# Kernel optimization log

Hardware: AMD Instinct MI355X
Metric: run time of the kernel (lower is better)

## Reference

```python
import jax, jax.numpy as jnp
import numpy as np

D_MODEL = 2048
NUM_HEADS = 16
NUM_KV_HEADS = 4
HEAD_DIM = D_MODEL // NUM_HEADS  # 128
B, T = 2, 2048


def setup_inputs() -> dict:
    key = jax.random.key(0)
    ks = jax.random.split(key, 9)
    d_kv = NUM_KV_HEADS * HEAD_DIM
    s = 1.0 / np.sqrt(D_MODEL)
    return {
        "x": jax.random.normal(ks[0], (B, T, D_MODEL), dtype=jnp.float32),
        "Wq": jax.random.normal(ks[1], (D_MODEL, D_MODEL), dtype=jnp.float32) * s,
        "bq": jnp.zeros((D_MODEL,), dtype=jnp.float32),
        "Wk": jax.random.normal(ks[2], (D_MODEL, d_kv), dtype=jnp.float32) * s,
        "bk": jnp.zeros((d_kv,), dtype=jnp.float32),
        "Wv": jax.random.normal(ks[3], (D_MODEL, d_kv), dtype=jnp.float32) * s,
        "bv": jnp.zeros((d_kv,), dtype=jnp.float32),
        "Wo": jax.random.normal(ks[4], (D_MODEL, D_MODEL), dtype=jnp.float32) * s,
        "bo": jnp.zeros((D_MODEL,), dtype=jnp.float32),
    }


def reference(x, Wq, bq, Wk, bk, Wv, bv, Wo, bo):
    b, t, _ = x.shape
    # projections
    q = x @ Wq + bq                      # [B,T,D]
    k = x @ Wk + bk                      # [B,T,KVH*Dh]
    v = x @ Wv + bv
    q = q.reshape(b, t, NUM_HEADS, HEAD_DIM)      # [B,T,H,Dh]
    k = k.reshape(b, t, NUM_KV_HEADS, HEAD_DIM)   # [B,T,KVH,Dh]
    v = v.reshape(b, t, NUM_KV_HEADS, HEAD_DIM)
    repeat = NUM_HEADS // NUM_KV_HEADS
    k = jnp.repeat(k, repeat, axis=2)              # [B,T,H,Dh]
    v = jnp.repeat(v, repeat, axis=2)
    scores = jnp.einsum('bthd,bshd->bhts', q, k) / jnp.sqrt(
        jnp.asarray(HEAD_DIM, dtype=x.dtype))
    mask = jnp.tril(jnp.ones((t, t), dtype=x.dtype))
    # faithful to source: multiplicative mask plus large negative on masked
    scores = scores * mask - 1e10 * (1.0 - mask)
    probs = jax.nn.softmax(scores, axis=-1)        # [B,H,T,S]
    out = jnp.einsum('bhts,bshd->bthd', probs, v)  # [B,T,H,Dh]
    out = out.reshape(b, t, NUM_HEADS * HEAD_DIM)  # merge heads
    return out @ Wo + bo                           # [B,T,D]
```

## Files before the change

### kernel.cpp

```cpp
#include <hip/hip_runtime.h>

typedef __attribute__((ext_vector_type(8))) __bf16 bf16x8;
typedef __attribute__((ext_vector_type(4))) float f32x4;
typedef __attribute__((ext_vector_type(4))) short short4v;

#define MFMA16(a,b,c)  __builtin_amdgcn_mfma_f32_16x16x32_bf16((a),(b),(c),0,0,0)
#define MFMA16K(a,b,c) __builtin_amdgcn_mfma_f32_16x16x16bf16_1k((a),(b),(c),0,0,0)

__device__ __forceinline__ short f2bf(float f){
  union { float f; unsigned u; } x; x.f = f;
  return (short)((x.u + 0x7fffu + ((x.u >> 16) & 1u)) >> 16);
}
__device__ __forceinline__ unsigned bits(float f){
  union { float f; unsigned u; } x; x.f = f; return x.u;
}

__device__ __forceinline__ void gld16(void* lds, const void* g){
  __builtin_amdgcn_global_load_lds(
      (const __attribute__((address_space(1))) unsigned*)g,
      (__attribute__((address_space(3))) unsigned*)lds, 16, 0, 0);
}


__global__ __launch_bounds__(256) void k_cvt8(const float* __restrict__ x,
                                              short* __restrict__ xb){
  long i = (long)blockIdx.x * 256 + threadIdx.x;
  const float4* xv = (const float4*)x;
  float4 a = xv[2*i], c = xv[2*i+1];
  short s[8] = {f2bf(a.x),f2bf(a.y),f2bf(a.z),f2bf(a.w),
                f2bf(c.x),f2bf(c.y),f2bf(c.z),f2bf(c.w)};
  *(uint4*)&xb[8*i] = *(uint4*)s;
}

__global__ void k_wt(const float* __restrict__ W, short* __restrict__ Wt, int N){
  __shared__ float tile[32][33];
  int tx = threadIdx.x, ty = threadIdx.y;
  int k0 = blockIdx.y*32, n0 = blockIdx.x*32;
  for (int j=0;j<32;j+=8)
    tile[ty+j][tx] = W[(size_t)(k0+ty+j)*N + n0 + tx];
  __syncthreads();
  for (int j=0;j<32;j+=8)
    Wt[(size_t)(n0+ty+j)*2048 + k0 + tx] = f2bf(tile[tx][ty+j]);
}

__global__ void k_bias(const float* __restrict__ bq, const float* __restrict__ bk,
                       const float* __restrict__ bv, float* __restrict__ outb){
  int i = blockIdx.x*256 + threadIdx.x;
  float v = (i < 2048) ? bq[i] : (i < 2560 ? bk[i-2048] : bv[i-2560]);
  outb[i] = v;
}

__global__ void k_vt(const short* __restrict__ qkv, short* __restrict__ Vt){
  __shared__ short tile[32][33];
  int tx = threadIdx.x, ty = threadIdx.y;
  int t0 = blockIdx.x*32, c0 = blockIdx.y*32;
  for (int j=0;j<32;j+=8)
    tile[ty+j][tx] = qkv[(size_t)(t0+ty+j)*3072 + 2560 + c0 + tx];
  __syncthreads();
  int b = t0 >> 11, t_in_b = t0 & 2047;
  for (int j=0;j<32;j+=8){
    int col = c0 + ty + j;
    int kvh = col >> 7, d = col & 127;
    Vt[((size_t)((b*4 + kvh)*128 + d))*2048 + t_in_b + tx] = tile[tx][ty+j];
  }
}

template<int OUT_BF16>
__global__ __launch_bounds__(256) void gemm_bt(const short* __restrict__ A,
    const short* __restrict__ Bt, const float* __restrict__ bias,
    void* __restrict__ Cv, int M, int N, int K){
  __shared__ short As[128*32];
  __shared__ short Bs[128*32];
  const int tid = threadIdx.x;
  const int w = tid >> 6, lane = tid & 63, l15 = lane & 15, quad = lane >> 4;
  const int wr = w >> 1, wc = w & 1;
  const int nbx = gridDim.x;
  const int lin = blockIdx.y * nbx + blockIdx.x;
  const int cpx = (nbx * gridDim.y) >> 3;
  const int swz = (lin & 7) * cpx + (lin >> 3);
  const int m0 = (swz / nbx) * 128, n0 = (swz % nbx) * 128;
  const int lrow = lane >> 2, lcol = (lane & 3)*8;
  const short* Ag = A  + (size_t)(m0 + w*32 + lrow)*K + lcol;
  const short* Bg = Bt + (size_t)(n0 + w*32 + lrow)*K + lcol;
  short* AsW0 = &As[(w*32)*32];
  short* AsW1 = &As[(w*32+16)*32];
  short* BsW0 = &Bs[(w*32)*32];
  short* BsW1 = &Bs[(w*32+16)*32];
  const size_t r16K = (size_t)16*K;
  f32x4 acc[4][4] = {};
  for (int kt = 0; kt < K; kt += 32){
    gld16(AsW0, Ag + kt);
    gld16(AsW1, Ag + kt + r16K);
    gld16(BsW0, Bg + kt);
    gld16(BsW1, Bg + kt + r16K);
    __syncthreads();
    bf16x8 af[4], bfr[4];
#pragma unroll
    for (int i=0;i<4;i++){
      af[i]  = *(const bf16x8*)&As[(wr*64 + i*16 + l15)*32 + quad*8];
      bfr[i] = *(const bf16x8*)&Bs[(wc*64 + i*16 + l15)*32 + quad*8];
    }
#pragma unroll
    for (int mi=0;mi<4;mi++)
#pragma unroll
      for (int nj=0;nj<4;nj++)
        acc[mi][nj] = MFMA16(af[mi], bfr[nj], acc[mi][nj]);
    __syncthreads();
  }
  float bv[4];
#pragma unroll
  for (int nj=0;nj<4;nj++) bv[nj] = bias[n0 + wc*64 + nj*16 + l15];
#pragma unroll
  for (int mi=0;mi<4;mi++){
    int row = m0 + wr*64 + mi*16 + quad*4;
#pragma unroll
    for (int nj=0;nj<4;nj++){
      int col = n0 + wc*64 + nj*16 + l15;
#pragma unroll
      for (int r=0;r<4;r++){
        float v = acc[mi][nj][r] + bv[nj];
        if (OUT_BF16) ((short*)Cv)[(size_t)(row+r)*N + col] = f2bf(v);
        else          ((float*)Cv)[(size_t)(row+r)*N + col] = v;
      }
    }
  }
}

__global__ __launch_bounds__(256) void k_attn(const short* __restrict__ qkv,
                                              const short* __restrict__ Vt,
                                              short* __restrict__ attn){
  constexpr float COEF = 0.12752365f;
  __shared__ short SM[16384];
  const int tid = threadIdx.x, w = tid >> 6, lane = tid & 63;
  const int l15 = lane & 15, quad = lane >> 4;
  const int p = blockIdx.x, h = blockIdx.y, b = blockIdx.z, kvh = h >> 2;

  const short* kb[2];
  const short* vb[2];
#pragma unroll
  for (int j=0;j<2;j++){
    int rK = w*8 + j*4 + (lane >> 4);
    int cK = (lane & 15) ^ (rK & 15);
    kb[j] = qkv + (size_t)(b*2048 + rK)*3072 + 2048 + kvh*128 + cK*8;
    int dV = w*32 + j*16 + (lane >> 2);
    int cV = (lane & 3) ^ (dV & 3) ^ ((dV >> 2) & 3);
    vb[j] = Vt + ((size_t)((b*4 + kvh)*128 + dV))*2048 + cV*8;
  }
  short* K0 = &SM[w*1024];
  short* V0 = &SM[4096 + w*1024];

  int buf = 0;
#pragma unroll
  for (int j=0;j<2;j++){
    gld16(K0 + j*512, kb[j]);
    gld16(V0 + j*512, vb[j]);
  }

  for (int sp = 0; sp < 2; sp++){
    const int qi = sp ? (31 - p) : p;
    const int qw = qi*64 + w*16;
    bf16x8 qf[4];
    {
      const short* qbase = qkv + ((size_t)(b*2048 + qw + l15))*3072 + h*128 + quad*8;
#pragma unroll
      for (int d4=0;d4<4;d4++)
        qf[d4] = *(const bf16x8*)(qbase + d4*32);
    }
    f32x4 accO[8] = {};
    float lsum = 0.f;
    const int nst = 2*qi + 2;

    for (int st = 0; st < nst; st++){
      __syncthreads();
      const int cur = buf;
      const int nb = buf ^ 1;
      {
        int nxt = -1;
        if (st + 1 < nst) nxt = (st + 1) * 32;
        else if (sp == 0) nxt = 0;
        if (nxt >= 0){
          short* Kd = &SM[nb*8192 + w*1024];
          short* Vd = &SM[nb*8192 + 4096 + w*1024];
          const size_t ko = (size_t)nxt * 3072;
#pragma unroll
          for (int j=0;j<2;j++){
            gld16(Kd + j*512, kb[j] + ko);
            gld16(Vd + j*512, vb[j] + nxt);
          }
        }
      }
      const int s0 = st * 32;
      if (s0 <= qw + 15){
        const short* Kb = &SM[cur*8192];
        const short* Vb = &SM[cur*8192 + 4096];
        bf16x8 kf[2][4];
#pragma unroll
        for (int ss=0;ss<2;ss++)
#pragma unroll
          for (int d4=0;d4<4;d4++){
            int slot = (ss*16 + l15)*16 + ((d4*4 + quad) ^ l15);
            kf[ss][d4] = *(const bf16x8*)&Kb[slot*8];
          }
        f32x4 sa[2] = {};
        __builtin_amdgcn_s_setprio(1);
#pragma unroll
        for (int d4=0;d4<4;d4++){
          sa[0] = MFMA16(kf[0][d4], qf[d4], sa[0]);
          sa[1] = MFMA16(kf[1][d4], qf[d4], sa[1]);
        }
        __builtin_amdgcn_s_setprio(0);
        short4v pf[2];
        const bool mneed = (s0 + 31 > qw);
        const int qgl = qw + l15;
#pragma unroll
        for (int sub=0;sub<2;sub++){
          float pr[4];
#pragma unroll
          for (int r=0;r<4;r++){
            float e = __builtin_amdgcn_exp2f(sa[sub][r] * COEF);
            int sg = s0 + sub*16 + quad*4 + r;
            if (mneed && (sg > qgl)) e = 0.f;
            pr[r] = e;
          }
          lsum += (pr[0]+pr[1]) + (pr[2]+pr[3]);
          union { unsigned u[2]; short4v s; } pk;
          pk.u[0] = __builtin_amdgcn_perm(bits(pr[1]), bits(pr[0]), 0x07060302u);
          pk.u[1] = __builtin_amdgcn_perm(bits(pr[3]), bits(pr[2]), 0x07060302u);
          pf[sub] = pk.s;
        }
        __builtin_amdgcn_s_setprio(1);
#pragma unroll
        for (int sub=0;sub<2;sub++)
#pragma unroll
          for (int dt=0;dt<8;dt++){
            int slot = (dt*16 + l15)*4 +
                       ((sub*2 + (quad>>1)) ^ (l15 & 3) ^ ((l15 >> 2) & 3));
            short4v vf = *(const short4v*)&Vb[slot*8 + (quad&1)*4];
            accO[dt] = MFMA16K(vf, pf[sub], accO[dt]);
          }
        __builtin_amdgcn_s_setprio(0);
      }
      buf = nb;
    }
    {
      float s = lsum;
      s += __shfl_xor(s, 16);
      s += __shfl_xor(s, 32);
      float inv = 1.0f / s;
      short* obase = attn + ((size_t)(b*2048 + qw + l15))*2048 + h*128 + quad*4;
#pragma unroll
      for (int dt=0;dt<8;dt++){
        float o0 = accO[dt][0]*inv, o1 = accO[dt][1]*inv;
        float o2 = accO[dt][2]*inv, o3 = accO[dt][3]*inv;
        union { unsigned u[2]; short4v s; } ok;
        ok.u[0] = __builtin_amdgcn_perm(bits(o1), bits(o0), 0x07060302u);
        ok.u[1] = __builtin_amdgcn_perm(bits(o3), bits(o2), 0x07060302u);
        *(short4v*)(obase + dt*16) = ok.s;
      }
    }
  }
}

extern "C" void kernel_launch(void* const* d_in, const int* in_sizes, int n_in,
                              void* d_out, int out_size, void* d_ws, size_t ws_size,
                              hipStream_t stream){
  const float* x  = (const float*)d_in[0];
  const float* Wq = (const float*)d_in[1];
  const float* bq = (const float*)d_in[2];
  const float* Wk = (const float*)d_in[3];
  const float* bk = (const float*)d_in[4];
  const float* Wv = (const float*)d_in[5];
  const float* bv = (const float*)d_in[6];
  const float* Wo = (const float*)d_in[7];
  const float* bo = (const float*)d_in[8];
  float* out = (float*)d_out;
  char* ws = (char*)d_ws;

  short* xb    = (short*)(ws + 0);
  short* WtQKV = (short*)(ws + (size_t)16*1024*1024);
  short* WoT   = (short*)(ws + (size_t)28*1024*1024);
  float* biasQ = (float*)(ws + (size_t)36*1024*1024);
  short* qkv   = (short*)(ws + (size_t)37*1024*1024);
  short* Vt    = (short*)(ws + (size_t)61*1024*1024);
  short* attn  = (short*)(ws + 0);

  k_cvt8<<<4096, 256, 0, stream>>>(x, xb);
  k_wt<<<dim3(64,64), dim3(32,8), 0, stream>>>(Wq, WtQKV, 2048);
  k_wt<<<dim3(16,64), dim3(32,8), 0, stream>>>(Wk, WtQKV + (size_t)2048*2048, 512);
  k_wt<<<dim3(16,64), dim3(32,8), 0, stream>>>(Wv, WtQKV + (size_t)2560*2048, 512);
  k_wt<<<dim3(64,64), dim3(32,8), 0, stream>>>(Wo, WoT, 2048);
  k_bias<<<12, 256, 0, stream>>>(bq, bk, bv, biasQ);
  gemm_bt<1><<<dim3(24,32), 256, 0, stream>>>(xb, WtQKV, biasQ, qkv, 4096, 3072, 2048);
  k_vt<<<dim3(128,16), dim3(32,8), 0, stream>>>(qkv, Vt);
  k_attn<<<dim3(16,16,2), 256, 0, stream>>>(qkv, Vt, attn);
  gemm_bt<0><<<dim3(16,32), 256, 0, stream>>>(attn, WoT, bo, out, 4096, 2048, 2048);
}
```

Before: 336.2 us.

## Replace GEMM with 256x256-tile, 8-wave, double-buffered pipelined kernel

Replaces the 128x128 synchronous-load GEMM with a 256x256 tile kernel using 512 threads. It double-buffers 64-wide K slices in 128 KB of LDS with an XOR-swizzled layout, and interleaves async global-to-LDS loads with MFMA phases using explicit vmcnt waits, barriers and setprio. The goal is to hide memory latency and raise data reuse per tile. The trade-off is fewer blocks (192 and 128) than CUs, which may leave part of the GPU idle.

```diff
diff --git a/kernel.cpp b/kernel.cpp
--- a/kernel.cpp
+++ b/kernel.cpp
@@ -19,6 +19,14 @@
   __builtin_amdgcn_global_load_lds(
       (const __attribute__((address_space(1))) unsigned*)g,
       (__attribute__((address_space(3))) unsigned*)lds, 16, 0, 0);
+}
+
+template<int N>
+__device__ __forceinline__ void s_wait_vmcnt(){
+  if constexpr (N==8)      asm volatile("s_waitcnt vmcnt(8)" ::: "memory");
+  else if constexpr (N==6) asm volatile("s_waitcnt vmcnt(6)" ::: "memory");
+  else if constexpr (N==4) asm volatile("s_waitcnt vmcnt(4)" ::: "memory");
+  else                     asm volatile("s_waitcnt vmcnt(0)" ::: "memory");
 }
 
 
@@ -66,59 +74,111 @@
 }
 
 template<int OUT_BF16>
-__global__ __launch_bounds__(256) void gemm_bt(const short* __restrict__ A,
+__global__ __launch_bounds__(512, 2) void gemm8(const short* __restrict__ A,
     const short* __restrict__ Bt, const float* __restrict__ bias,
     void* __restrict__ Cv, int M, int N, int K){
-  __shared__ short As[128*32];
-  __shared__ short Bs[128*32];
+  __shared__ short SM[65536];
   const int tid = threadIdx.x;
   const int w = tid >> 6, lane = tid & 63, l15 = lane & 15, quad = lane >> 4;
-  const int wr = w >> 1, wc = w & 1;
-  const int nbx = gridDim.x;
-  const int lin = blockIdx.y * nbx + blockIdx.x;
-  const int cpx = (nbx * gridDim.y) >> 3;
-  const int swz = (lin & 7) * cpx + (lin >> 3);
-  const int m0 = (swz / nbx) * 128, n0 = (swz % nbx) * 128;
-  const int lrow = lane >> 2, lcol = (lane & 3)*8;
-  const short* Ag = A  + (size_t)(m0 + w*32 + lrow)*K + lcol;
-  const short* Bg = Bt + (size_t)(n0 + w*32 + lrow)*K + lcol;
-  short* AsW0 = &As[(w*32)*32];
-  short* AsW1 = &As[(w*32+16)*32];
-  short* BsW0 = &Bs[(w*32)*32];
-  short* BsW1 = &Bs[(w*32+16)*32];
-  const size_t r16K = (size_t)16*K;
-  f32x4 acc[4][4] = {};
-  for (int kt = 0; kt < K; kt += 32){
-    gld16(AsW0, Ag + kt);
-    gld16(AsW1, Ag + kt + r16K);
-    gld16(BsW0, Bg + kt);
-    gld16(BsW1, Bg + kt + r16K);
-    __syncthreads();
-    bf16x8 af[4], bfr[4];
-#pragma unroll
-    for (int i=0;i<4;i++){
-      af[i]  = *(const bf16x8*)&As[(wr*64 + i*16 + l15)*32 + quad*8];
-      bfr[i] = *(const bf16x8*)&Bs[(wc*64 + i*16 + l15)*32 + quad*8];
-    }
-#pragma unroll
-    for (int mi=0;mi<4;mi++)
-#pragma unroll
-      for (int nj=0;nj<4;nj++)
-        acc[mi][nj] = MFMA16(af[mi], bfr[nj], acc[mi][nj]);
-    __syncthreads();
-  }
-  float bv[4];
-#pragma unroll
-  for (int nj=0;nj<4;nj++) bv[nj] = bias[n0 + wc*64 + nj*16 + l15];
-#pragma unroll
-  for (int mi=0;mi<4;mi++){
-    int row = m0 + wr*64 + mi*16 + quad*4;
-#pragma unroll
-    for (int nj=0;nj<4;nj++){
-      int col = n0 + wc*64 + nj*16 + l15;
+  const int wr = w >> 2, wc = w & 3;
+  const int m0 = blockIdx.y * 256, n0 = blockIdx.x * 256;
+  const int ln8 = lane >> 3;
+  const int g8 = (((lane & 7) ^ (ln8 & 7)) << 3);
+  const short* aB = A  + (size_t)(m0 + w*16 + ln8) * K + g8;
+  const short* bB = Bt + (size_t)(n0 + w*16 + ln8) * K + g8;
+  const int aRB = (wr*64 + l15)*64;
+  const int bRB = (wc*32 + l15)*64;
+  const int phys0 = (((quad    ) ^ (l15 & 7)) << 3);
+  const int phys1 = (((quad + 4) ^ (l15 & 7)) << 3);
+  f32x4 acc[2][4][2][2] = {};
+  bf16x8 aF[4][2], bLo[2][2], bHi[2][2];
+  const int nt = K >> 6;
+
+#define STG_A(bufi, Ah, T)  do{ \
+    short* d_ = &SM[(bufi)*32768 + ((Ah)*128 + w*16)*64]; \
+    const short* s_ = aB + (size_t)((Ah)*128)*K + (size_t)(T)*64; \
+    gld16(d_,      s_); \
+    gld16(d_+512,  s_ + (size_t)8*K); }while(0)
+#define STG_B(bufi, Bh, T)  do{ \
+    short* d_ = &SM[(bufi)*32768 + 16384 + ((Bh)*128 + w*16)*64]; \
+    const short* s_ = bB + (size_t)((Bh)*128)*K + (size_t)(T)*64; \
+    gld16(d_,      s_); \
+    gld16(d_+512,  s_ + (size_t)8*K); }while(0)
+#define RD_A(bufi, Ah) do{ \
+    const short* p_ = &SM[(bufi)*32768 + ((Ah)*128)*64 + aRB]; \
+    _Pragma("unroll") for(int m_=0;m_<4;m_++){ \
+      aF[m_][0] = *(const bf16x8*)&p_[m_*1024 + phys0]; \
+      aF[m_][1] = *(const bf16x8*)&p_[m_*1024 + phys1]; } }while(0)
+#define RD_B(bufi, Bh, dst) do{ \
+    const short* p_ = &SM[(bufi)*32768 + 16384 + ((Bh)*128)*64 + bRB]; \
+    _Pragma("unroll") for(int n_=0;n_<2;n_++){ \
+      dst[n_][0] = *(const bf16x8*)&p_[n_*1024 + phys0]; \
+      dst[n_][1] = *(const bf16x8*)&p_[n_*1024 + phys1]; } }while(0)
+#define MM(Ah, Bh, bsrc) do{ __builtin_amdgcn_s_setprio(1); \
+    _Pragma("unroll") for(int m_=0;m_<4;m_++) \
+    _Pragma("unroll") for(int n_=0;n_<2;n_++){ \
+      acc[Ah][m_][Bh][n_] = MFMA16(aF[m_][0], bsrc[n_][0], acc[Ah][m_][Bh][n_]); \
+      acc[Ah][m_][Bh][n_] = MFMA16(aF[m_][1], bsrc[n_][1], acc[Ah][m_][Bh][n_]); } \
+    __builtin_amdgcn_s_setprio(0); }while(0)
+#define GROUP(T, STHI, STLO, W1, W2) do{ \
+    const int c_ = (T)&1, nc_ = c_^1; \
+    s_wait_vmcnt<W1>(); \
+    __builtin_amdgcn_s_barrier(); \
+    __builtin_amdgcn_sched_barrier(0); \
+    if (STHI) STG_A(nc_, 1, (T)+1); \
+    RD_A(c_, 0); RD_B(c_, 0, bLo); \
+    MM(0, 0, bLo); \
+    s_wait_vmcnt<W2>(); \
+    __builtin_amdgcn_s_barrier(); \
+    __builtin_amdgcn_sched_barrier(0); \
+    if (STHI) STG_B(nc_, 1, (T)+1); \
+    RD_B(c_, 1, bHi); \
+    MM(0, 1, bHi); \
+    __builtin_amdgcn_s_barrier(); \
+    __builtin_amdgcn_sched_barrier(0); \
+    if (STLO) STG_A(c_, 0, (T)+2); \
+    RD_A(c_, 1); \
+    MM(1, 0, bLo); \
+    __builtin_amdgcn_s_barrier(); \
+    __builtin_amdgcn_sched_barrier(0); \
+    if (STLO) STG_B(c_, 0, (T)+2); \
+    MM(1, 1, bHi); \
+  }while(0)
+
+  STG_A(0, 0, 0); STG_B(0, 0, 0);
+  STG_A(0, 1, 0); STG_B(0, 1, 0);
+  STG_A(1, 0, 1); STG_B(1, 0, 1);
+
+  for (int T = 0; T < nt-2; ++T) GROUP(T, true, true, 8, 6);
+  GROUP(nt-2, true,  false, 8, 6);
+  GROUP(nt-1, false, false, 4, 0);
+
+#undef GROUP
+#undef MM
+#undef RD_B
+#undef RD_A
+#undef STG_B
+#undef STG_A
+
+  float bv[2][2];
+#pragma unroll
+  for (int Bh=0;Bh<2;Bh++)
+#pragma unroll
+    for (int n=0;n<2;n++)
+      bv[Bh][n] = bias[n0 + Bh*128 + wc*32 + n*16 + l15];
+#pragma unroll
+  for (int Ah=0;Ah<2;Ah++)
+#pragma unroll
+  for (int m=0;m<4;m++){
+    int row = m0 + Ah*128 + wr*64 + m*16 + quad*4;
+#pragma unroll
+    for (int Bh=0;Bh<2;Bh++)
+#pragma unroll
+    for (int n=0;n<2;n++){
+      int col = n0 + Bh*128 + wc*32 + n*16 + l15;
 #pragma unroll
       for (int r=0;r<4;r++){
-        float v = acc[mi][nj][r] + bv[nj];
+        float v = acc[Ah][m][Bh][n][r] + bv[Bh][n];
         if (OUT_BF16) ((short*)Cv)[(size_t)(row+r)*N + col] = f2bf(v);
         else          ((float*)Cv)[(size_t)(row+r)*N + col] = v;
       }
@@ -290,8 +350,8 @@
   k_wt<<<dim3(16,64), dim3(32,8), 0, stream>>>(Wv, WtQKV + (size_t)2560*2048, 512);
   k_wt<<<dim3(64,64), dim3(32,8), 0, stream>>>(Wo, WoT, 2048);
   k_bias<<<12, 256, 0, stream>>>(bq, bk, bv, biasQ);
-  gemm_bt<1><<<dim3(24,32), 256, 0, stream>>>(xb, WtQKV, biasQ, qkv, 4096, 3072, 2048);
+  gemm8<1><<<dim3(12,16), 512, 0, stream>>>(xb, WtQKV, biasQ, qkv, 4096, 3072, 2048);
   k_vt<<<dim3(128,16), dim3(32,8), 0, stream>>>(qkv, Vt);
   k_attn<<<dim3(16,16,2), 256, 0, stream>>>(qkv, Vt, attn);
-  gemm_bt<0><<<dim3(16,32), 256, 0, stream>>>(attn, WoT, bo, out, 4096, 2048, 2048);
-}
+  gemm8<0><<<dim3(8,16), 512, 0, stream>>>(attn, WoT, bo, out, 4096, 2048, 2048);
+}
```

Measured after the change: 313.2 us. -6.9%, faster.

## Replace projection GEMMs with double-buffered, swizzled, multi-chunk 512-thread GEMM

Applied to the files above, without the earlier changes.

Replaces the simple single-buffered 128x128 GEMM with a 512-thread kernel. Each block computes a 128x(BCH*128) tile with a K-step of 64, keeps two LDS buffers, and issues global-to-LDS prefetch of the next tiles using explicit vmcnt waits and barriers. LDS rows use XOR swizzling to avoid bank conflicts, and MFMA sections raise wave priority. The aim is to hide global load latency and reuse A tiles across several B chunks, at the cost of more LDS, hand-tuned wait counts that must match the load ordering, and the removal of the L2 block swizzle.

```diff
diff --git a/kernel.cpp b/kernel.cpp
--- a/kernel.cpp
+++ b/kernel.cpp
@@ -19,6 +19,15 @@
   __builtin_amdgcn_global_load_lds(
       (const __attribute__((address_space(1))) unsigned*)g,
       (__attribute__((address_space(3))) unsigned*)lds, 16, 0, 0);
+}
+
+template<int N>
+__device__ __forceinline__ void s_wait_vmcnt(){
+  if constexpr (N==8)      asm volatile("s_waitcnt vmcnt(8)" ::: "memory");
+  else if constexpr (N==6) asm volatile("s_waitcnt vmcnt(6)" ::: "memory");
+  else if constexpr (N==4) asm volatile("s_waitcnt vmcnt(4)" ::: "memory");
+  else if constexpr (N==2) asm volatile("s_waitcnt vmcnt(2)" ::: "memory");
+  else                     asm volatile("s_waitcnt vmcnt(0)" ::: "memory");
 }
 
 
@@ -65,60 +74,106 @@
   }
 }
 
-template<int OUT_BF16>
-__global__ __launch_bounds__(256) void gemm_bt(const short* __restrict__ A,
+template<int BCH, int OUT_BF16>
+__global__ __launch_bounds__(512, 2) void gemmR(const short* __restrict__ A,
     const short* __restrict__ Bt, const float* __restrict__ bias,
-    void* __restrict__ Cv, int M, int N, int K){
-  __shared__ short As[128*32];
-  __shared__ short Bs[128*32];
+    void* __restrict__ Cv, int N, int K){
+  constexpr int ASZ  = 8192;
+  constexpr int BUFS = ASZ*(1+BCH);
+  __shared__ short SM[2*BUFS];
   const int tid = threadIdx.x;
   const int w = tid >> 6, lane = tid & 63, l15 = lane & 15, quad = lane >> 4;
-  const int wr = w >> 1, wc = w & 1;
-  const int nbx = gridDim.x;
-  const int lin = blockIdx.y * nbx + blockIdx.x;
-  const int cpx = (nbx * gridDim.y) >> 3;
-  const int swz = (lin & 7) * cpx + (lin >> 3);
-  const int m0 = (swz / nbx) * 128, n0 = (swz % nbx) * 128;
-  const int lrow = lane >> 2, lcol = (lane & 3)*8;
-  const short* Ag = A  + (size_t)(m0 + w*32 + lrow)*K + lcol;
-  const short* Bg = Bt + (size_t)(n0 + w*32 + lrow)*K + lcol;
-  short* AsW0 = &As[(w*32)*32];
-  short* AsW1 = &As[(w*32+16)*32];
-  short* BsW0 = &Bs[(w*32)*32];
-  short* BsW1 = &Bs[(w*32+16)*32];
-  const size_t r16K = (size_t)16*K;
-  f32x4 acc[4][4] = {};
-  for (int kt = 0; kt < K; kt += 32){
-    gld16(AsW0, Ag + kt);
-    gld16(AsW1, Ag + kt + r16K);
-    gld16(BsW0, Bg + kt);
-    gld16(BsW1, Bg + kt + r16K);
-    __syncthreads();
-    bf16x8 af[4], bfr[4];
-#pragma unroll
-    for (int i=0;i<4;i++){
-      af[i]  = *(const bf16x8*)&As[(wr*64 + i*16 + l15)*32 + quad*8];
-      bfr[i] = *(const bf16x8*)&Bs[(wc*64 + i*16 + l15)*32 + quad*8];
-    }
-#pragma unroll
-    for (int mi=0;mi<4;mi++)
-#pragma unroll
-      for (int nj=0;nj<4;nj++)
-        acc[mi][nj] = MFMA16(af[mi], bfr[nj], acc[mi][nj]);
-    __syncthreads();
-  }
-  float bv[4];
-#pragma unroll
-  for (int nj=0;nj<4;nj++) bv[nj] = bias[n0 + wc*64 + nj*16 + l15];
-#pragma unroll
-  for (int mi=0;mi<4;mi++){
-    int row = m0 + wr*64 + mi*16 + quad*4;
-#pragma unroll
-    for (int nj=0;nj<4;nj++){
-      int col = n0 + wc*64 + nj*16 + l15;
-#pragma unroll
-      for (int r=0;r<4;r++){
-        float v = acc[mi][nj][r] + bv[nj];
+  const int wr = w >> 2, wc = w & 3;
+  const int m0 = blockIdx.y * 128, n0 = blockIdx.x * (BCH*128);
+  const int ln8 = lane >> 3;
+  const int g8 = (((lane & 7) ^ ln8) << 3);
+  const short* aB = A  + (size_t)(m0 + w*16 + ln8) * K + g8;
+  const short* bB = Bt + (size_t)(n0 + w*16 + ln8) * K + g8;
+  const int aRB = (wr*64 + l15)*64;
+  const int bRB = (wc*32 + l15)*64;
+  const int phys0 = ((quad     ^ (l15 & 7)) << 3);
+  const int phys1 = (((quad+4) ^ (l15 & 7)) << 3);
+  f32x4 acc[BCH][4][2] = {};
+  bf16x8 aF[4][2], bF[2][2];
+  const int nt = K >> 6;
+
+#define STG_A(bufi, T) do{ \
+    short* d_ = &SM[(bufi)*BUFS + w*1024]; \
+    const short* s_ = aB + (size_t)(T)*64; \
+    gld16(d_, s_); gld16(d_+512, s_ + (size_t)8*K); }while(0)
+#define STG_B(bufi, ch, T) do{ \
+    short* d_ = &SM[(bufi)*BUFS + ASZ + (ch)*ASZ + w*1024]; \
+    const short* s_ = bB + (size_t)((ch)*128)*K + (size_t)(T)*64; \
+    gld16(d_, s_); gld16(d_+512, s_ + (size_t)8*K); }while(0)
+#define RD_A(bufi) do{ const short* p_ = &SM[(bufi)*BUFS + aRB]; \
+    _Pragma("unroll") for(int m_=0;m_<4;m_++){ \
+      aF[m_][0] = *(const bf16x8*)&p_[m_*1024 + phys0]; \
+      aF[m_][1] = *(const bf16x8*)&p_[m_*1024 + phys1]; } }while(0)
+#define RD_B(bufi, ch) do{ const short* p_ = &SM[(bufi)*BUFS + ASZ + (ch)*ASZ + bRB]; \
+    _Pragma("unroll") for(int n_=0;n_<2;n_++){ \
+      bF[n_][0] = *(const bf16x8*)&p_[n_*1024 + phys0]; \
+      bF[n_][1] = *(const bf16x8*)&p_[n_*1024 + phys1]; } }while(0)
+#define MM(ch) do{ __builtin_amdgcn_s_setprio(1); \
+    _Pragma("unroll") for(int m_=0;m_<4;m_++) \
+    _Pragma("unroll") for(int n_=0;n_<2;n_++){ \
+      acc[ch][m_][n_] = MFMA16(aF[m_][0], bF[n_][0], acc[ch][m_][n_]); \
+      acc[ch][m_][n_] = MFMA16(aF[m_][1], bF[n_][1], acc[ch][m_][n_]); } \
+    __builtin_amdgcn_s_setprio(0); }while(0)
+#define PH(W) do{ s_wait_vmcnt<W>(); \
+    __builtin_amdgcn_s_barrier(); \
+    __builtin_amdgcn_sched_barrier(0); }while(0)
+#define GROUP3(T, ST1, ST2, W0, W1, W2) do{ \
+    const int c_=(T)&1, n_c=c_^1; \
+    PH(W0); if (ST1) STG_B(n_c,1,(T)+1); RD_A(c_); RD_B(c_,0); MM(0); \
+    PH(W1); if (ST1) STG_B(n_c,2,(T)+1); RD_B(c_,1); MM(1); \
+    PH(W2); if (ST2){ STG_A(c_,(T)+2); STG_B(c_,0,(T)+2); } RD_B(c_,2); MM(2); \
+  }while(0)
+#define GROUP2(T, ST1, ST2, W0, W1) do{ \
+    const int c_=(T)&1, n_c=c_^1; \
+    PH(W0); if (ST1) STG_B(n_c,1,(T)+1); RD_A(c_); RD_B(c_,0); MM(0); \
+    PH(W1); if (ST2){ STG_A(c_,(T)+2); STG_B(c_,0,(T)+2); } RD_B(c_,1); MM(1); \
+  }while(0)
+
+  if constexpr (BCH == 3){
+    STG_A(0,0); STG_B(0,0,0); STG_B(0,1,0); STG_B(0,2,0);
+    STG_A(1,1); STG_B(1,0,1);
+    for (int T = 0; T < nt-2; ++T) GROUP3(T, true, true, 8,8,8);
+    GROUP3(nt-2, true,  false, 8,8,8);
+    GROUP3(nt-1, false, false, 4,2,0);
+  } else {
+    STG_A(0,0); STG_B(0,0,0); STG_B(0,1,0);
+    STG_A(1,1); STG_B(1,0,1);
+    for (int T = 0; T < nt-2; ++T) GROUP2(T, true, true, 6,6);
+    GROUP2(nt-2, true,  false, 6,6);
+    GROUP2(nt-1, false, false, 2,0);
+  }
+
+#undef GROUP2
+#undef GROUP3
+#undef PH
+#undef MM
+#undef RD_B
+#undef RD_A
+#undef STG_B
+#undef STG_A
+
+  float bv[BCH][2];
+#pragma unroll
+  for (int ch=0; ch<BCH; ch++)
+#pragma unroll
+    for (int n=0; n<2; n++)
+      bv[ch][n] = bias[n0 + ch*128 + wc*32 + n*16 + l15];
+#pragma unroll
+  for (int ch=0; ch<BCH; ch++)
+#pragma unroll
+  for (int m=0; m<4; m++){
+    int row = m0 + wr*64 + m*16 + quad*4;
+#pragma unroll
+    for (int n=0; n<2; n++){
+      int col = n0 + ch*128 + wc*32 + n*16 + l15;
+#pragma unroll
+      for (int r=0; r<4; r++){
+        float v = acc[ch][m][n][r] + bv[ch][n];
         if (OUT_BF16) ((short*)Cv)[(size_t)(row+r)*N + col] = f2bf(v);
         else          ((float*)Cv)[(size_t)(row+r)*N + col] = v;
       }
@@ -290,8 +345,8 @@
   k_wt<<<dim3(16,64), dim3(32,8), 0, stream>>>(Wv, WtQKV + (size_t)2560*2048, 512);
   k_wt<<<dim3(64,64), dim3(32,8), 0, stream>>>(Wo, WoT, 2048);
   k_bias<<<12, 256, 0, stream>>>(bq, bk, bv, biasQ);
-  gemm_bt<1><<<dim3(24,32), 256, 0, stream>>>(xb, WtQKV, biasQ, qkv, 4096, 3072, 2048);
+  gemmR<3,1><<<dim3(8,32), 512, 0, stream>>>(xb, WtQKV, biasQ, qkv, 3072, 2048);
   k_vt<<<dim3(128,16), dim3(32,8), 0, stream>>>(qkv, Vt);
   k_attn<<<dim3(16,16,2), 256, 0, stream>>>(qkv, Vt, attn);
-  gemm_bt<0><<<dim3(16,32), 256, 0, stream>>>(attn, WoT, bo, out, 4096, 2048, 2048);
-}
+  gemmR<2,0><<<dim3(8,32), 512, 0, stream>>>(attn, WoT, bo, out, 2048, 2048);
+}
```

Result: faster. 293.6 us (-12.7%).
